# Kernel tuning notes

Measured on AMD Instinct MI355X. Metric: run time of the kernel, lower is better.

The kernel has to match this reference:

```python
import jax, jax.numpy as jnp
import numpy as np

N_NODES = 100000
N_EDGES = 1600000
N_GRAPHS = 2000
IN_DIM, HID, OUT_DIM, N_CLS = 6, 256, 128, 60
EPS = 1e-5


def setup_inputs() -> dict:
    key = jax.random.key(0)
    ks = jax.random.split(key, 16)
    def lin(k, i, o):
        s = 1.0 / np.sqrt(i)
        k1, k2 = jax.random.split(k)
        return (jax.random.uniform(k1, (i, o), jnp.float32, -s, s),
                jax.random.uniform(k2, (o,), jnp.float32, -s, s))
    W_emb, b_emb = lin(ks[0], IN_DIM, HID)
    Wc1, bc1 = lin(ks[1], HID, HID)
    W2, b2 = lin(ks[2], HID, HID)
    Wc2, bc2 = lin(ks[3], HID, HID)
    W3, b3 = lin(ks[4], HID, OUT_DIM)
    Wcls, bcls = lin(ks[5], OUT_DIM, N_CLS)
    return {
        'node_features': jax.random.normal(ks[6], (N_NODES, IN_DIM), jnp.float32),
        'src': jax.random.randint(ks[7], (N_EDGES,), 0, N_NODES, jnp.int32),
        'dst': jax.random.randint(ks[8], (N_EDGES,), 0, N_NODES, jnp.int32),
        'graph_ids': jnp.sort(jax.random.randint(ks[9], (N_NODES,), 0, N_GRAPHS, jnp.int32)),
        'W_emb': W_emb, 'b_emb': b_emb,
        'Wc1': Wc1, 'bc1': bc1,
        'g1': jnp.ones((HID,), jnp.float32), 'be1': jnp.zeros((HID,), jnp.float32),
        'W2': W2, 'b2': b2,
        'Wc2': Wc2, 'bc2': bc2,
        'g2': jnp.ones((HID,), jnp.float32), 'be2': jnp.zeros((HID,), jnp.float32),
        'W3': W3, 'b3': b3,
        'Wcls': Wcls, 'bcls': bcls,
    }


def _graph_conv(x, W, b, src, dst, dout_isqrt, din_isqrt):
    # DGL GraphConv, norm='both': msg = x_src * dout^-1/2, sum to dst, * din^-1/2, then W, b
    m = x[src] * dout_isqrt[src][:, None]            # [E, H]
    agg = jax.ops.segment_sum(m, dst, num_segments=N_NODES)
    agg = agg * din_isqrt[:, None]
    return agg @ W + b


def _bn(h, g, b):
    # BatchNorm1d, training mode: batch stats over node dim, biased variance
    mu = jnp.mean(h, axis=0)
    var = jnp.mean(jnp.square(h - mu), axis=0)
    return (h - mu) * jax.lax.rsqrt(var + EPS) * g + b


def reference(node_features, src, dst, graph_ids, W_emb, b_emb, Wc1, bc1, g1, be1,
              W2, b2, Wc2, bc2, g2, be2, W3, b3, Wcls, bcls):
    ones_e = jnp.ones((N_EDGES,), jnp.float32)
    dout = jax.ops.segment_sum(ones_e, src, num_segments=N_NODES)
    din = jax.ops.segment_sum(ones_e, dst, num_segments=N_NODES)
    dout_isqrt = jnp.where(dout > 0, jax.lax.rsqrt(jnp.maximum(dout, 1.0)), 0.0)
    din_isqrt = jnp.where(din > 0, jax.lax.rsqrt(jnp.maximum(din, 1.0)), 0.0)

    x = node_features @ W_emb + b_emb                              # [N, H]
    h = x + _graph_conv(x, Wc1, bc1, src, dst, dout_isqrt, din_isqrt)
    h = jax.nn.relu(_bn(h, g1, be1))
    h = h @ W2 + b2
    h = x + _graph_conv(h, Wc2, bc2, src, dst, dout_isqrt, din_isqrt)
    h = jax.nn.relu(_bn(h, g2, be2))
    h = h @ W3 + b3                                                # [N, OUT_DIM]

    # dgl.mean_nodes: per-graph mean of h
    sums = jax.ops.segment_sum(h, graph_ids, num_segments=N_GRAPHS)
    cnts = jax.ops.segment_sum(jnp.ones((N_NODES,), jnp.float32), graph_ids, num_segments=N_GRAPHS)
    y = sums / jnp.maximum(cnts, 1.0)[:, None]                     # [G, OUT_DIM]
    label = y @ Wcls + bcls                                        # [G, N_CLS]
    return h, label
```

## Files before the change

### kernel.cpp

```cpp
#include <hip/hip_runtime.h>

#define NNODES 100000
#define MPAD   100032
#define NEDGES 1600000
#define NGRAPHS 2000
#define HID 256
#define OUTD 128
#define NCLS 60
#define BN_EPS 1e-5f
#define NROWBLK 1563
#define NSCANBLK 98
#define REDBLK 32
#define DPAD 16

typedef __attribute__((ext_vector_type(8))) short bf16x8;
typedef __attribute__((ext_vector_type(4))) float f32x4;

__device__ __forceinline__ float b2f(unsigned short b) {
    unsigned int u = ((unsigned int)b) << 16;
    return __builtin_bit_cast(float, u);
}
__device__ __forceinline__ unsigned short f2b(float f) {
    unsigned int u = __builtin_bit_cast(unsigned int, f);
    u = (u + 0x7FFFu + ((u >> 16) & 1u)) >> 16;
    return (unsigned short)u;
}

__global__ void k_zero4(int4* __restrict__ p, int n4) {
    int i = blockIdx.x * blockDim.x + threadIdx.x;
    if (i < n4) p[i] = make_int4(0, 0, 0, 0);
}

__global__ __launch_bounds__(256) void k_deg2(
        const int* __restrict__ src, const int* __restrict__ dst,
        int* __restrict__ dout, int* __restrict__ din, int* __restrict__ lpos) {
    int t = blockIdx.x * 256 + threadIdx.x;
#pragma unroll
    for (int j = 0; j < 4; ++j) {
        int e = t + j * 400128;
        if (e < NEDGES) {
            atomicAdd(&dout[src[e] * DPAD], 1);
            lpos[e] = atomicAdd(&din[dst[e] * DPAD], 1);
        }
    }
}

__global__ void k_blk_sum(const int* __restrict__ din, const int* __restrict__ dout,
                          int* __restrict__ bsum, float* __restrict__ dos,
                          float* __restrict__ dis) {
    __shared__ int red[256];
    int blk = blockIdx.x, tid = threadIdx.x;
    int base = blk * 1024;
    int s = 0;
#pragma unroll
    for (int j = 0; j < 4; ++j) {
        int i = base + tid + j * 256;
        if (i < NNODES) {
            int b = din[i * DPAD];
            int a = dout[i * DPAD];
            s += b;
            dos[i] = a > 0 ? 1.0f / sqrtf((float)a) : 0.0f;
            dis[i] = b > 0 ? 1.0f / sqrtf((float)b) : 0.0f;
        }
    }
    red[tid] = s;
    __syncthreads();
    for (int off = 128; off > 0; off >>= 1) {
        if (tid < off) red[tid] += red[tid + off];
        __syncthreads();
    }
    if (tid == 0) bsum[blk] = red[0];
}

__global__ void k_scan_bsum(int* __restrict__ bsum) {
    if (threadIdx.x == 0) {
        int acc = 0;
        for (int i = 0; i < NSCANBLK; ++i) { int v = bsum[i]; bsum[i] = acc; acc += v; }
    }
}

__global__ void k_scan_local(const int* __restrict__ deg, const int* __restrict__ bsum,
                             int* __restrict__ row_ptr) {
    __shared__ int buf[1024];
    int blk = blockIdx.x, tid = threadIdx.x;
    int i = blk * 1024 + tid;
    int v = (i < NNODES) ? deg[i * DPAD] : 0;
    buf[tid] = v;
    __syncthreads();
    for (int off = 1; off < 1024; off <<= 1) {
        int t = (tid >= off) ? buf[tid - off] : 0;
        __syncthreads();
        buf[tid] += t;
        __syncthreads();
    }
    int inc = buf[tid] + bsum[blk];
    if (i < NNODES) row_ptr[i + 1] = inc;
    if (i == 0) row_ptr[0] = 0;
}

__global__ void k_place(const int* __restrict__ src, const int* __restrict__ dst,
                        const int* __restrict__ lpos, const int* __restrict__ row_ptr,
                        int* __restrict__ csr_e) {
    int e = blockIdx.x * blockDim.x + threadIdx.x;
    if (e < NEDGES) csr_e[row_ptr[dst[e]] + lpos[e]] = src[e];
}

__global__ void k_prep(const float* __restrict__ nf, const float* __restrict__ dos,
                       float* __restrict__ nf7,
                       const float* __restrict__ W2, const float* __restrict__ Wc2,
                       const float* __restrict__ W3, unsigned short* __restrict__ Wt2,
                       unsigned short* __restrict__ Wtc2, unsigned short* __restrict__ Wt3,
                       const float* __restrict__ Wemb, const float* __restrict__ bemb,
                       const float* __restrict__ Wc1, float* __restrict__ M1,
                       float* __restrict__ v1) {
    int blk = blockIdx.x, tid = threadIdx.x;
    if (blk < 391) {
        int n = blk * 256 + tid;
        if (n < NNODES) {
            float w = dos[n];
            const float* p = nf + (size_t)n * 6;
            float4 lo = {p[0] * w, p[1] * w, p[2] * w, p[3] * w};
            float4 hi = {p[4] * w, p[5] * w, w, 0.f};
            float4* o = (float4*)(nf7 + (size_t)n * 8);
            o[0] = lo; o[1] = hi;
        }
    } else if (blk < 1031) {
        int idx = (blk - 391) * 256 + tid;
        if (idx < 65536) {
            int n = idx >> 8, k = idx & 255;
            Wt2[idx] = f2b(W2[k * 256 + n]);
        } else if (idx < 131072) {
            int j = idx - 65536;
            int n = j >> 8, k = j & 255;
            Wtc2[j] = f2b(Wc2[k * 256 + n]);
        } else {
            int j = idx - 131072;
            int n = j >> 8, k = j & 255;
            Wt3[j] = f2b(W3[k * 128 + n]);
        }
    } else {
        int bi = blk - 1031;
        int c = tid;
        float acc = 0.f;
        if (bi < 6) {
            for (int k = 0; k < HID; ++k) acc = fmaf(Wemb[bi * HID + k], Wc1[k * HID + c], acc);
            M1[bi * HID + c] = acc;
        } else {
            for (int k = 0; k < HID; ++k) acc = fmaf(bemb[k], Wc1[k * HID + c], acc);
            v1[c] = acc;
        }
    }
}

__global__ void k_agg6(const int* __restrict__ row_ptr, const int* __restrict__ csr_e,
                       const float* __restrict__ nf7, float* __restrict__ t7) {
    int n = blockIdx.x * blockDim.x + threadIdx.x;
    if (n >= NNODES) return;
    float a0 = 0, a1 = 0, a2 = 0, a3 = 0, a4 = 0, a5 = 0, a6 = 0;
    int s = row_ptr[n], e = row_ptr[n + 1];
    int i = s;
    for (; i + 2 <= e; i += 2) {
        const float4* p0 = (const float4*)(nf7 + (size_t)csr_e[i] * 8);
        const float4* p1 = (const float4*)(nf7 + (size_t)csr_e[i + 1] * 8);
        float4 l0 = p0[0], h0 = p0[1], l1 = p1[0], h1 = p1[1];
        a0 += l0.x; a1 += l0.y; a2 += l0.z; a3 += l0.w; a4 += h0.x; a5 += h0.y; a6 += h0.z;
        a0 += l1.x; a1 += l1.y; a2 += l1.z; a3 += l1.w; a4 += h1.x; a5 += h1.y; a6 += h1.z;
    }
    if (i < e) {
        const float4* p0 = (const float4*)(nf7 + (size_t)csr_e[i] * 8);
        float4 l0 = p0[0], h0 = p0[1];
        a0 += l0.x; a1 += l0.y; a2 += l0.z; a3 += l0.w; a4 += h0.x; a5 += h0.y; a6 += h0.z;
    }
    float4* o = (float4*)(t7 + (size_t)n * 8);
    o[0] = make_float4(a0, a1, a2, a3);
    o[1] = make_float4(a4, a5, a6, 0.f);
}

__global__ __launch_bounds__(256) void k_layer1(
    const float* __restrict__ nf, const float* __restrict__ Wemb, const float* __restrict__ bemb,
    const float* __restrict__ M1, const float* __restrict__ v1, const float* __restrict__ bc1,
    const float* __restrict__ t7, const float* __restrict__ dis,
    unsigned short* __restrict__ H, float* __restrict__ psum, float* __restrict__ psq) {
    __shared__ float s_nf[64][6];
    __shared__ float s_t7[64][8];
    __shared__ float s_r[64];
    int blk = blockIdx.x;
    int n0 = blk * 64;
    int tid = threadIdx.x;
    for (int t = tid; t < 384; t += 256) {
        int nl = t / 6, i = t % 6;
        int n = n0 + nl;
        s_nf[nl][i] = (n < NNODES) ? nf[(size_t)n * 6 + i] : 0.f;
    }
    if (tid < 128) {
        int n = n0 + tid / 2;
        if (n < NNODES)
            ((float4*)s_t7)[tid] = ((const float4*)(t7 + (size_t)n0 * 8))[tid];
        else
            ((float4*)s_t7)[tid] = make_float4(0.f, 0.f, 0.f, 0.f);
    }
    if (tid < 64) {
        int n = n0 + tid;
        s_r[tid] = (n < NNODES) ? dis[n] : 0.f;
    }
    int c = tid;
    float wc[6], mc[6];
#pragma unroll
    for (int i = 0; i < 6; ++i) { wc[i] = Wemb[i * HID + c]; mc[i] = M1[i * HID + c]; }
    float v1c = v1[c];
    float bsum = bemb[c] + bc1[c];
    __syncthreads();
    float ps = 0.f, pq = 0.f;
    int nmax = min(64, NNODES - n0);
    for (int nl = 0; nl < nmax; ++nl) {
        float nfd = 0.f, td = 0.f;
#pragma unroll
        for (int i = 0; i < 6; ++i) {
            nfd = fmaf(s_nf[nl][i], wc[i], nfd);
            td = fmaf(s_t7[nl][i], mc[i], td);
        }
        float val = nfd + s_r[nl] * (td + s_t7[nl][6] * v1c) + bsum;
        H[(size_t)(n0 + nl) * HID + c] = f2b(val);
        ps += val;
        pq = fmaf(val, val, pq);
    }
    for (int nl = nmax; nl < 64; ++nl) H[(size_t)(n0 + nl) * HID + c] = 0;
    psum[blk * HID + c] = ps;
    psq[blk * HID + c] = pq;
}

__global__ void k_bn_part(const float* __restrict__ psum, const float* __restrict__ psq,
                          double* __restrict__ tmp) {
    int c = threadIdx.x;
    int s = blockIdx.x;
    double a = 0.0, b = 0.0;
    for (int bb = s; bb < NROWBLK; bb += REDBLK) {
        a += psum[bb * HID + c];
        b += psq[bb * HID + c];
    }
    tmp[s * HID + c] = a;
    tmp[(REDBLK + s) * HID + c] = b;
}

__global__ void k_bn_final(const double* __restrict__ tmp, const float* __restrict__ g,
                           const float* __restrict__ be, float* __restrict__ scale,
                           float* __restrict__ shift) {
    int c = threadIdx.x;
    double s = 0.0, q = 0.0;
    for (int i = 0; i < REDBLK; ++i) { s += tmp[i * HID + c]; q += tmp[(REDBLK + i) * HID + c]; }
    double mu = s / (double)NNODES;
    double var = q / (double)NNODES - mu * mu;
    if (var < 0.0) var = 0.0;
    double inv = 1.0 / sqrt(var + (double)BN_EPS);
    float sc = (float)((double)g[c] * inv);
    scale[c] = sc;
    shift[c] = be[c] - (float)mu * sc;
}

template <int NC, bool ATRANS, bool XEPI, bool PART, bool OUTF32, bool RS>
__global__ __launch_bounds__(256, 2) void k_mgemm(
    const unsigned short* __restrict__ A, const unsigned short* __restrict__ Bt,
    const float* __restrict__ bias,
    const float* __restrict__ scale, const float* __restrict__ shift,
    const float* __restrict__ nf, const float* __restrict__ Wemb, const float* __restrict__ bemb,
    const float* __restrict__ rs,
    unsigned short* __restrict__ Cb, float* __restrict__ Cf,
    float* __restrict__ psum, float* __restrict__ psq) {
    __shared__ unsigned short As[64 * 256];
    __shared__ unsigned short Bs[64 * 256];
    __shared__ float sSc[HID];
    __shared__ float sSh[HID];
    __shared__ float sNf[64][6];
    __shared__ float sXW[6][HID];
    __shared__ float sRs[64];
    __shared__ float redS[2][64];
    __shared__ float redQ[2][64];

    int tid = threadIdx.x;
    int rb = blockIdx.x;
    int row0 = rb * 64;

    if (ATRANS) { sSc[tid] = scale[tid]; sSh[tid] = shift[tid]; }
    if (RS && tid < 64) {
        int n = row0 + tid;
        sRs[tid] = (n < NNODES) ? rs[n] : 0.f;
    }
    if (XEPI) {
        for (int t = tid; t < 6 * NC; t += 256) {
            int i = t / NC, cl = t % NC;
            sXW[i][cl] = Wemb[i * HID + cl];
        }
        if (tid < 64) {
            int n = row0 + tid;
#pragma unroll
            for (int i = 0; i < 6; ++i) sNf[tid][i] = (n < NNODES) ? nf[(size_t)n * 6 + i] : 0.f;
        }
    }
    if (ATRANS) __syncthreads();

#pragma unroll
    for (int i = 0; i < 8; ++i) {
        int g = i * 256 + tid;
        int row = g >> 5, kc = g & 31;
        uint4 v = *(const uint4*)(A + (size_t)(row0 + row) * 256 + kc * 8);
        if (ATRANS) {
            unsigned int w[4] = {v.x, v.y, v.z, v.w};
#pragma unroll
            for (int q = 0; q < 4; ++q) {
                int k0 = kc * 8 + q * 2;
                float f0 = b2f((unsigned short)(w[q] & 0xffffu));
                float f1 = b2f((unsigned short)(w[q] >> 16));
                f0 = fmaxf(fmaf(f0, sSc[k0], sSh[k0]), 0.f);
                f1 = fmaxf(fmaf(f1, sSc[k0 + 1], sSh[k0 + 1]), 0.f);
                w[q] = (unsigned int)f2b(f0) | ((unsigned int)f2b(f1) << 16);
            }
            v.x = w[0]; v.y = w[1]; v.z = w[2]; v.w = w[3];
        }
        int pkc = kc ^ (row & 7);
        *(uint4*)(&As[row * 256 + pkc * 8]) = v;
    }

    int w = tid >> 6, lane = tid & 63;
    int wm = w >> 1, wn = w & 1;
    int lrow = lane & 15, lk = lane >> 4;

    for (int cb = 0; cb < NC / 64; ++cb) {
        int c0 = cb * 64;
        if (cb) __syncthreads();
#pragma unroll
        for (int i = 0; i < 8; ++i) {
            int g = i * 256 + tid;
            int row = g >> 5, kc = g & 31;
            uint4 v = *(const uint4*)(Bt + (size_t)(c0 + row) * 256 + kc * 8);
            int pkc = kc ^ (row & 7);
            *(uint4*)(&Bs[row * 256 + pkc * 8]) = v;
        }
        __syncthreads();

        f32x4 acc[2][2] = {};
#pragma unroll
        for (int ks = 0; ks < 8; ++ks) {
            bf16x8 af[2], bfr[2];
#pragma unroll
            for (int fm = 0; fm < 2; ++fm) {
                int r = wm * 32 + fm * 16 + lrow;
                int kc = ks * 4 + lk;
                af[fm] = *(const bf16x8*)(&As[r * 256 + (kc ^ (r & 7)) * 8]);
            }
#pragma unroll
            for (int fn = 0; fn < 2; ++fn) {
                int r = wn * 32 + fn * 16 + lrow;
                int kc = ks * 4 + lk;
                bfr[fn] = *(const bf16x8*)(&Bs[r * 256 + (kc ^ (r & 7)) * 8]);
            }
#pragma unroll
            for (int fm = 0; fm < 2; ++fm)
#pragma unroll
                for (int fn = 0; fn < 2; ++fn)
                    acc[fm][fn] = __builtin_amdgcn_mfma_f32_16x16x32_bf16(af[fm], bfr[fn], acc[fm][fn], 0, 0, 0);
        }

        float pS[2] = {0.f, 0.f}, pQ[2] = {0.f, 0.f};
#pragma unroll
        for (int fn = 0; fn < 2; ++fn) {
            int cl = wn * 32 + fn * 16 + lrow;
            int gc = c0 + cl;
            float bv = bias[gc];
            if (XEPI) bv += bemb[gc];
#pragma unroll
            for (int fm = 0; fm < 2; ++fm) {
#pragma unroll
                for (int r = 0; r < 4; ++r) {
                    int rl = wm * 32 + fm * 16 + lk * 4 + r;
                    int gr = row0 + rl;
                    float val = acc[fm][fn][r] + bv;
                    if (XEPI) {
#pragma unroll
                        for (int l = 0; l < 6; ++l) val = fmaf(sNf[rl][l], sXW[l][gc], val);
                    }
                    if (RS) val *= sRs[rl];
                    if (gr < NNODES) {
                        if (OUTF32) Cf[(size_t)gr * NC + gc] = val;
                        else        Cb[(size_t)gr * NC + gc] = f2b(val);
                        if (PART) { pS[fn] += val; pQ[fn] = fmaf(val, val, pQ[fn]); }
                    }
                }
            }
        }
        if (PART) {
#pragma unroll
            for (int fn = 0; fn < 2; ++fn) {
                float s = pS[fn], q = pQ[fn];
                s += __shfl_xor(s, 16); s += __shfl_xor(s, 32);
                q += __shfl_xor(q, 16); q += __shfl_xor(q, 32);
                if (lk == 0) {
                    int cl = wn * 32 + fn * 16 + lrow;
                    redS[wm][cl] = s;
                    redQ[wm][cl] = q;
                }
            }
            __syncthreads();
            if (tid < 64) {
                psum[(size_t)rb * HID + c0 + tid] = redS[0][tid] + redS[1][tid];
                psq [(size_t)rb * HID + c0 + tid] = redQ[0][tid] + redQ[1][tid];
            }
        }
    }
}

#define ADD8(vv) { \
    a[0] += b2f((unsigned short)(vv.x & 0xffffu)); \
    a[1] += b2f((unsigned short)(vv.x >> 16)); \
    a[2] += b2f((unsigned short)(vv.y & 0xffffu)); \
    a[3] += b2f((unsigned short)(vv.y >> 16)); \
    a[4] += b2f((unsigned short)(vv.z & 0xffffu)); \
    a[5] += b2f((unsigned short)(vv.z >> 16)); \
    a[6] += b2f((unsigned short)(vv.w & 0xffffu)); \
    a[7] += b2f((unsigned short)(vv.w >> 16)); }

__global__ __launch_bounds__(256) void k_agg(const int* __restrict__ row_ptr,
                                             const int* __restrict__ csr_e,
                                             const unsigned short* __restrict__ X,
                                             const float* __restrict__ dis,
                                             unsigned short* __restrict__ out) {
    int wid = threadIdx.x >> 6, lane = threadIdx.x & 63;
    int half = lane >> 5, l32 = lane & 31;
    int n = blockIdx.x * 4 + wid;
    if (n >= NNODES) return;
    int s = row_ptr[n], e = row_ptr[n + 1];
    float a[8] = {0.f, 0.f, 0.f, 0.f, 0.f, 0.f, 0.f, 0.f};
    int i = s;
    for (; i + 8 <= e; i += 8) {
        int s0 = csr_e[i + half];
        int s1 = csr_e[i + 2 + half];
        int s2 = csr_e[i + 4 + half];
        int s3 = csr_e[i + 6 + half];
        uint4 v0 = ((const uint4*)(X + (size_t)s0 * HID))[l32];
        uint4 v1 = ((const uint4*)(X + (size_t)s1 * HID))[l32];
        uint4 v2 = ((const uint4*)(X + (size_t)s2 * HID))[l32];
        uint4 v3 = ((const uint4*)(X + (size_t)s3 * HID))[l32];
        ADD8(v0) ADD8(v1) ADD8(v2) ADD8(v3)
    }
    for (; i + 2 <= e; i += 2) {
        int s0 = csr_e[i + half];
        uint4 v0 = ((const uint4*)(X + (size_t)s0 * HID))[l32];
        ADD8(v0)
    }
    if (i < e && half == 0) {
        int s0 = csr_e[i];
        uint4 v0 = ((const uint4*)(X + (size_t)s0 * HID))[l32];
        ADD8(v0)
    }
#pragma unroll
    for (int j = 0; j < 8; ++j) a[j] += __shfl_xor(a[j], 32);
    if (half == 0) {
        float r = dis[n];
        uint4 o;
        o.x = (unsigned)f2b(a[0] * r) | ((unsigned)f2b(a[1] * r) << 16);
        o.y = (unsigned)f2b(a[2] * r) | ((unsigned)f2b(a[3] * r) << 16);
        o.z = (unsigned)f2b(a[4] * r) | ((unsigned)f2b(a[5] * r) << 16);
        o.w = (unsigned)f2b(a[6] * r) | ((unsigned)f2b(a[7] * r) << 16);
        ((uint4*)(out + (size_t)n * HID))[l32] = o;
    }
}

__global__ __launch_bounds__(128) void k_mean_label(const float* __restrict__ Hout,
                                                    const int* __restrict__ gids,
                                                    const float* __restrict__ Wcls,
                                                    const float* __restrict__ bcls,
                                                    float* __restrict__ lab) {
    int g = blockIdx.x;
    int c = threadIdx.x;
    int lo = 0, hi = NNODES;
    while (lo < hi) { int mid = (lo + hi) >> 1; if (gids[mid] < g) lo = mid + 1; else hi = mid; }
    int s = lo;
    hi = NNODES;
    while (lo < hi) { int mid = (lo + hi) >> 1; if (gids[mid] < g + 1) lo = mid + 1; else hi = mid; }
    int e = lo;
    float acc = 0.f;
    for (int n = s; n < e; ++n) acc += Hout[(size_t)n * OUTD + c];
    int cnt = e - s;
    float y = acc / (float)max(cnt, 1);
    __shared__ float ys[OUTD];
    ys[c] = y;
    __syncthreads();
    if (c < NCLS) {
        float a = bcls[c];
        for (int k = 0; k < OUTD; ++k) a = fmaf(ys[k], Wcls[k * NCLS + c], a);
        lab[(size_t)g * NCLS + c] = a;
    }
}

extern "C" void kernel_launch(void* const* d_in, const int* in_sizes, int n_in,
                              void* d_out, int out_size, void* d_ws, size_t ws_size,
                              hipStream_t stream) {
    const float* nf   = (const float*)d_in[0];
    const int*   src  = (const int*)d_in[1];
    const int*   dst  = (const int*)d_in[2];
    const int*   gids = (const int*)d_in[3];
    const float* Wemb = (const float*)d_in[4];
    const float* bemb = (const float*)d_in[5];
    const float* Wc1  = (const float*)d_in[6];
    const float* bc1  = (const float*)d_in[7];
    const float* g1   = (const float*)d_in[8];
    const float* be1  = (const float*)d_in[9];
    const float* W2   = (const float*)d_in[10];
    const float* b2   = (const float*)d_in[11];
    const float* Wc2  = (const float*)d_in[12];
    const float* bc2  = (const float*)d_in[13];
    const float* g2   = (const float*)d_in[14];
    const float* be2  = (const float*)d_in[15];
    const float* W3   = (const float*)d_in[16];
    const float* b3   = (const float*)d_in[17];
    const float* Wcls = (const float*)d_in[18];
    const float* bcls = (const float*)d_in[19];

    float* out_h   = (float*)d_out;
    float* out_lab = out_h + (size_t)NNODES * OUTD;

    float* ws = (float*)d_ws;
    size_t off = 0;
    auto take = [&](size_t n) { float* p = ws + off; off += (n + 63) & ~(size_t)63; return p; };
    unsigned short* actA = (unsigned short*)take((size_t)MPAD * HID / 2);
    unsigned short* actB = (unsigned short*)take((size_t)MPAD * HID / 2);
    unsigned short* Wt2  = (unsigned short*)take(HID * HID / 2);
    unsigned short* Wtc2 = (unsigned short*)take(HID * HID / 2);
    unsigned short* Wt3  = (unsigned short*)take(OUTD * HID / 2);
    float* dout_is = take(NNODES);
    float* din_is  = take(NNODES);
    int*   row_ptr = (int*)take(NNODES + 1);
    float* lpos_t7 = take(NEDGES);
    int*   csr_e   = (int*)take(NEDGES);
    float* nf7_ps  = take(800320);
    float* M1      = take(6 * HID);
    float* v1      = take(HID);
    float* scale1  = take(HID);
    float* shift1  = take(HID);
    float* scale2  = take(HID);
    float* shift2  = take(HID);
    int*   bsum    = (int*)take(128);
    double* bn_tmp = (double*)take(2 * 2 * REDBLK * HID);

    int*   deg_out = (int*)actA;
    int*   deg_in  = deg_out + 100032 * DPAD;
    int*   lpos    = (int*)lpos_t7;
    float* t7      = lpos_t7;
    float* nf7     = nf7_ps;
    float* psum    = nf7_ps;
    float* psq     = nf7_ps + 400128;

    k_zero4<<<(2 * 100032 * DPAD / 4 + 255) / 256, 256, 0, stream>>>(
        (int4*)deg_out, 2 * 100032 * DPAD / 4);
    k_deg2<<<1563, 256, 0, stream>>>(src, dst, deg_out, deg_in, lpos);
    k_blk_sum<<<NSCANBLK, 256, 0, stream>>>(deg_in, deg_out, bsum, dout_is, din_is);
    k_scan_bsum<<<1, 64, 0, stream>>>(bsum);
    k_scan_local<<<NSCANBLK, 1024, 0, stream>>>(deg_in, bsum, row_ptr);
    k_place<<<(NEDGES + 255) / 256, 256, 0, stream>>>(src, dst, lpos, row_ptr, csr_e);
    k_prep<<<1038, 256, 0, stream>>>(nf, dout_is, nf7, W2, Wc2, W3, Wt2, Wtc2, Wt3,
                                     Wemb, bemb, Wc1, M1, v1);
    k_agg6<<<(NNODES + 255) / 256, 256, 0, stream>>>(row_ptr, csr_e, nf7, t7);
    k_layer1<<<NROWBLK, 256, 0, stream>>>(nf, Wemb, bemb, M1, v1, bc1, t7, din_is,
                                          actA, psum, psq);
    k_bn_part<<<REDBLK, 256, 0, stream>>>(psum, psq, bn_tmp);
    k_bn_final<<<1, 256, 0, stream>>>(bn_tmp, g1, be1, scale1, shift1);
    k_mgemm<HID, true, false, false, false, true><<<NROWBLK, 256, 0, stream>>>(
        actA, Wt2, b2, scale1, shift1, nullptr, nullptr, nullptr, dout_is,
        actB, nullptr, nullptr, nullptr);
    k_agg<<<NNODES / 4, 256, 0, stream>>>(row_ptr, csr_e, actB, din_is, actA);
    k_mgemm<HID, false, true, true, false, false><<<NROWBLK, 256, 0, stream>>>(
        actA, Wtc2, bc2, nullptr, nullptr, nf, Wemb, bemb, nullptr,
        actB, nullptr, psum, psq);
    k_bn_part<<<REDBLK, 256, 0, stream>>>(psum, psq, bn_tmp);
    k_bn_final<<<1, 256, 0, stream>>>(bn_tmp, g2, be2, scale2, shift2);
    k_mgemm<OUTD, true, false, false, true, false><<<NROWBLK, 256, 0, stream>>>(
        actB, Wt3, b3, scale2, shift2, nullptr, nullptr, nullptr, nullptr,
        nullptr, out_h, nullptr, nullptr);
    k_mean_label<<<NGRAPHS, OUTD, 0, stream>>>(out_h, gids, Wcls, bcls, out_lab);
}
```

Baseline: 723.1 us.

## Replace global-atomic degree counting with LDS-privatized chunked histograms for CSR build

Degree counting and per-edge rank assignment now use shared-memory histograms. Each block scans one edge slice and counts only the destinations (or sources) that fall in its 16K-node chunk, so the padded global atomics and the zeroing kernel are no longer needed. Per-slice partial counts are then prefix-summed across slices to give deterministic edge offsets, which the place kernel combines with row_ptr and the local rank. The trade-off is that every block rereads its whole edge slice once per chunk (7 chunks), and the partial arrays add extra global traffic.

```diff
diff --git a/kernel.cpp b/kernel.cpp
--- a/kernel.cpp
+++ b/kernel.cpp
@@ -11,7 +11,10 @@
 #define NROWBLK 1563
 #define NSCANBLK 98
 #define REDBLK 32
-#define DPAD 16
+#define CHUNK 16384
+#define NCHUNK 7
+#define NSLICE 32
+#define ESLICE 50000
 
 typedef __attribute__((ext_vector_type(8))) short bf16x8;
 typedef __attribute__((ext_vector_type(4))) float f32x4;
@@ -26,28 +29,65 @@
     return (unsigned short)u;
 }
 
-__global__ void k_zero4(int4* __restrict__ p, int n4) {
-    int i = blockIdx.x * blockDim.x + threadIdx.x;
-    if (i < n4) p[i] = make_int4(0, 0, 0, 0);
-}
-
-__global__ __launch_bounds__(256) void k_deg2(
+__global__ __launch_bounds__(256) void k_hist(
         const int* __restrict__ src, const int* __restrict__ dst,
-        int* __restrict__ dout, int* __restrict__ din, int* __restrict__ lpos) {
-    int t = blockIdx.x * 256 + threadIdx.x;
-#pragma unroll
-    for (int j = 0; j < 4; ++j) {
-        int e = t + j * 400128;
-        if (e < NEDGES) {
-            atomicAdd(&dout[src[e] * DPAD], 1);
-            lpos[e] = atomicAdd(&din[dst[e] * DPAD], 1);
-        }
-    }
-}
-
-__global__ void k_blk_sum(const int* __restrict__ din, const int* __restrict__ dout,
-                          int* __restrict__ bsum, float* __restrict__ dos,
-                          float* __restrict__ dis) {
+        int* __restrict__ partialD, int* __restrict__ partialS,
+        int* __restrict__ lrank) {
+    __shared__ int h[CHUNK];
+    int bid = blockIdx.x;
+    bool isD = bid < NCHUNK * NSLICE;
+    int id = isD ? bid : bid - NCHUNK * NSLICE;
+    int c = id / NSLICE, s = id % NSLICE;
+    int tid = threadIdx.x;
+    for (int i = tid; i < CHUNK; i += 256) h[i] = 0;
+    __syncthreads();
+    int e0 = s * ESLICE;
+    int lo = c * CHUNK;
+    if (isD) {
+#pragma unroll 4
+        for (int e = e0 + tid; e < e0 + ESLICE; e += 256) {
+            int d = dst[e];
+            unsigned int b = (unsigned int)(d - lo);
+            if (b < CHUNK) lrank[e] = atomicAdd(&h[b], 1);
+        }
+    } else {
+#pragma unroll 4
+        for (int e = e0 + tid; e < e0 + ESLICE; e += 256) {
+            int d = src[e];
+            unsigned int b = (unsigned int)(d - lo);
+            if (b < CHUNK) atomicAdd(&h[b], 1);
+        }
+    }
+    __syncthreads();
+    int* out = (isD ? partialD : partialS) + ((size_t)c * NSLICE + s) * CHUNK;
+    for (int i = tid; i < CHUNK; i += 256) out[i] = h[i];
+}
+
+__global__ __launch_bounds__(256) void k_sprefix(
+        int* __restrict__ partialD, const int* __restrict__ partialS,
+        int* __restrict__ din, float* __restrict__ dos, float* __restrict__ dis) {
+    int g = blockIdx.x * 256 + threadIdx.x;
+    int c = g >> 14, bin = g & (CHUNK - 1);
+    int acc = 0;
+#pragma unroll 4
+    for (int s = 0; s < NSLICE; ++s) {
+        size_t idx = ((size_t)c * NSLICE + s) * CHUNK + bin;
+        int v = partialD[idx];
+        partialD[idx] = acc;
+        acc += v;
+    }
+    int so = 0;
+#pragma unroll 4
+    for (int s = 0; s < NSLICE; ++s)
+        so += partialS[((size_t)c * NSLICE + s) * CHUNK + bin];
+    if (g < NNODES) {
+        din[g] = acc;
+        dos[g] = so > 0 ? rsqrtf((float)so) : 0.f;
+        dis[g] = acc > 0 ? rsqrtf((float)acc) : 0.f;
+    }
+}
+
+__global__ void k_blk_sum(const int* __restrict__ din, int* __restrict__ bsum) {
     __shared__ int red[256];
     int blk = blockIdx.x, tid = threadIdx.x;
     int base = blk * 1024;
@@ -55,13 +95,7 @@
 #pragma unroll
     for (int j = 0; j < 4; ++j) {
         int i = base + tid + j * 256;
-        if (i < NNODES) {
-            int b = din[i * DPAD];
-            int a = dout[i * DPAD];
-            s += b;
-            dos[i] = a > 0 ? 1.0f / sqrtf((float)a) : 0.0f;
-            dis[i] = b > 0 ? 1.0f / sqrtf((float)b) : 0.0f;
-        }
+        if (i < NNODES) s += din[i];
     }
     red[tid] = s;
     __syncthreads();
@@ -84,7 +118,7 @@
     __shared__ int buf[1024];
     int blk = blockIdx.x, tid = threadIdx.x;
     int i = blk * 1024 + tid;
-    int v = (i < NNODES) ? deg[i * DPAD] : 0;
+    int v = (i < NNODES) ? deg[i] : 0;
     buf[tid] = v;
     __syncthreads();
     for (int off = 1; off < 1024; off <<= 1) {
@@ -98,11 +132,17 @@
     if (i == 0) row_ptr[0] = 0;
 }
 
-__global__ void k_place(const int* __restrict__ src, const int* __restrict__ dst,
-                        const int* __restrict__ lpos, const int* __restrict__ row_ptr,
-                        int* __restrict__ csr_e) {
-    int e = blockIdx.x * blockDim.x + threadIdx.x;
-    if (e < NEDGES) csr_e[row_ptr[dst[e]] + lpos[e]] = src[e];
+__global__ __launch_bounds__(256) void k_place(
+        const int* __restrict__ src, const int* __restrict__ dst,
+        const int* __restrict__ lrank, const int* __restrict__ row_ptr,
+        const int* __restrict__ partialD, int* __restrict__ csr_e) {
+    int e = blockIdx.x * 256 + threadIdx.x;
+    if (e >= NEDGES) return;
+    int d = dst[e];
+    int s = e / ESLICE;
+    int c = d >> 14, bin = d & (CHUNK - 1);
+    int pos = row_ptr[d] + partialD[((size_t)c * NSLICE + s) * CHUNK + bin] + lrank[e];
+    csr_e[pos] = src[e];
 }
 
 __global__ void k_prep(const float* __restrict__ nf, const float* __restrict__ dos,
@@ -529,8 +569,9 @@
     float* dout_is = take(NNODES);
     float* din_is  = take(NNODES);
     int*   row_ptr = (int*)take(NNODES + 1);
-    float* lpos_t7 = take(NEDGES);
+    int*   din     = (int*)take(NNODES);
     int*   csr_e   = (int*)take(NEDGES);
+    float* t7      = take((size_t)MPAD * 8);
     float* nf7_ps  = take(800320);
     float* M1      = take(6 * HID);
     float* v1      = take(HID);
@@ -541,21 +582,21 @@
     int*   bsum    = (int*)take(128);
     double* bn_tmp = (double*)take(2 * 2 * REDBLK * HID);
 
-    int*   deg_out = (int*)actA;
-    int*   deg_in  = deg_out + 100032 * DPAD;
-    int*   lpos    = (int*)lpos_t7;
-    float* t7      = lpos_t7;
-    float* nf7     = nf7_ps;
-    float* psum    = nf7_ps;
-    float* psq     = nf7_ps + 400128;
-
-    k_zero4<<<(2 * 100032 * DPAD / 4 + 255) / 256, 256, 0, stream>>>(
-        (int4*)deg_out, 2 * 100032 * DPAD / 4);
-    k_deg2<<<1563, 256, 0, stream>>>(src, dst, deg_out, deg_in, lpos);
-    k_blk_sum<<<NSCANBLK, 256, 0, stream>>>(deg_in, deg_out, bsum, dout_is, din_is);
+    int*   partialD = (int*)actA;
+    int*   partialS = partialD + (size_t)NCHUNK * NSLICE * CHUNK;
+    int*   lrank    = (int*)actB;
+    float* nf7      = nf7_ps;
+    float* psum     = nf7_ps;
+    float* psq      = nf7_ps + 400128;
+
+    k_hist<<<2 * NCHUNK * NSLICE, 256, 0, stream>>>(src, dst, partialD, partialS, lrank);
+    k_sprefix<<<NCHUNK * CHUNK / 256, 256, 0, stream>>>(partialD, partialS, din,
+                                                        dout_is, din_is);
+    k_blk_sum<<<NSCANBLK, 256, 0, stream>>>(din, bsum);
     k_scan_bsum<<<1, 64, 0, stream>>>(bsum);
-    k_scan_local<<<NSCANBLK, 1024, 0, stream>>>(deg_in, bsum, row_ptr);
-    k_place<<<(NEDGES + 255) / 256, 256, 0, stream>>>(src, dst, lpos, row_ptr, csr_e);
+    k_scan_local<<<NSCANBLK, 1024, 0, stream>>>(din, bsum, row_ptr);
+    k_place<<<(NEDGES + 255) / 256, 256, 0, stream>>>(src, dst, lrank, row_ptr,
+                                                      partialD, csr_e);
     k_prep<<<1038, 256, 0, stream>>>(nf, dout_is, nf7, W2, Wc2, W3, Wt2, Wtc2, Wt3,
                                      Wemb, bemb, Wc1, M1, v1);
     k_agg6<<<(NNODES + 255) / 256, 256, 0, stream>>>(row_ptr, csr_e, nf7, t7);
```

Result: faster. 683.5 us (-5.5%).
